# Optimization experiments

Hardware: AMD Instinct MI355X
Metric: run time of the kernel (lower is better)

The kernel has to match this reference:

```python
import jax, jax.numpy as jnp
import numpy as np

# static config matching init_kwargs / setup
T = 0.1      # temperature
MARG = 0.0   # margin m
NEG_IOU = 0.5
K = 1        # pos_topk
WEIGHT = 1.0
P = 2080     # number of True entries in mask2d (triu of 64x64)


def _normalize(x, axis=-1, eps=1e-12):
    n = jnp.sqrt(jnp.sum(x * x, axis=axis, keepdims=True))
    return x / jnp.maximum(n, eps)


def _log_ce(pos_scores, all_scores, neg_mask, t, m):
    # pos_scores: (..., K); all_scores: (..., K or 1, L); neg_mask broadcastable to all_scores
    pos_logit = (pos_scores - m) / t
    pos_exp = jnp.exp(pos_logit)
    neg_exp_sum = jnp.sum(jnp.exp(all_scores / t) * neg_mask.astype(all_scores.dtype), axis=-1)
    loss = -(pos_logit - jnp.log(pos_exp + neg_exp_sum))
    return jnp.mean(loss)


def setup_inputs() -> dict:
    key = jax.random.key(0)
    k1, k2, k3, k4 = jax.random.split(key, 4)
    S, C, N, B, M = 64, 256, 64, 16, 128
    video_feats = jax.random.normal(k1, (S, C, N, N), dtype=jnp.float32)
    sents_feats = jax.random.normal(k2, (S, C), dtype=jnp.float32)
    iou2d = jax.random.uniform(k3, (S, N, N), dtype=jnp.float32)
    iou2ds = jax.random.uniform(k4, (M, N, N), dtype=jnp.float32)
    num_sentences = jnp.full((B,), 4, dtype=jnp.int32)   # sum == S
    num_targets = jnp.full((S,), 2, dtype=jnp.int32)     # sum == M
    mask2d = jnp.triu(jnp.ones((N, N), dtype=bool))      # P = 2080 valid proposals
    return {
        "video_feats": video_feats, "sents_feats": sents_feats,
        "iou2d": iou2d, "iou2ds": iou2ds,
        "num_sentences": num_sentences, "num_targets": num_targets,
        "mask2d": mask2d,
    }


def reference(video_feats, sents_feats, iou2d, iou2ds, num_sentences, num_targets, mask2d):
    S, C, N, _ = video_feats.shape
    B = num_sentences.shape[0]
    M = iou2ds.shape[0]

    # flat proposal indices (static count P)
    mask_idx = jnp.nonzero(mask2d.reshape(-1), size=P)[0]

    # scatter maps
    scatter_b2s = jnp.concatenate([jnp.zeros((1,), jnp.int32),
                                   jnp.cumsum(num_sentences)[:-1].astype(jnp.int32)])  # (B,)
    scatter_m2s = jnp.repeat(jnp.arange(S), num_targets, total_repeat_length=M)        # (M,)
    scatter_s2b = jnp.repeat(jnp.arange(B), num_sentences, total_repeat_length=S)      # (S,)

    # select valid proposals: (S,C,P) -> (S,P,C)
    vf = video_feats.reshape(S, C, N * N)[:, :, mask_idx].transpose(0, 2, 1)
    iou2d_f = iou2d.reshape(S, N * N)[:, mask_idx]    # (S,P)
    iou2ds_f = iou2ds.reshape(M, N * N)[:, mask_idx]  # (M,P)

    vf = _normalize(vf, axis=-1)          # (S,P,C)
    sf = _normalize(sents_feats, axis=-1) # (S,C)

    # top-K proposals per moment
    topk_idxs = jax.lax.top_k(iou2ds_f, K)[1]                         # (M,K)
    allm_vf = vf[scatter_m2s]                                         # (M,P,C)
    topk_vf = jnp.take_along_axis(allm_vf, topk_idxs[:, :, None], 1)  # (M,K,C)

    # inter-video loss
    inter_video_pos = jnp.sum(topk_vf * sf[scatter_m2s][:, None, :], axis=-1)  # (M,K)
    inter_video_all = jnp.einsum('mkc,sc->mks', topk_vf, sf)                   # (M,K,S)
    eye_mask = ~jnp.eye(S, dtype=bool)
    inter_video_neg_mask = eye_mask[scatter_m2s][:, None, :]                   # (M,1,S)
    loss_inter_video = _log_ce(inter_video_pos, inter_video_all, inter_video_neg_mask, T, MARG)

    # inter-query loss
    inter_query_pos = inter_video_pos                                  # (M,K)
    vf_b = vf[scatter_b2s].reshape(B * P, C)                           # one sentence-rep per video
    inter_query_all = jnp.einsum('sc,qc->sq', sf, vf_b)[:, None, :]    # (S,1,B*P)

    # pos_mask: row s has its video block b=scatter_s2b[s] set to (iou2d > neg_iou)
    s2v_pos = iou2d_f > NEG_IOU                                        # (S,P)
    pos_mask = jnp.zeros((S, B, P), dtype=bool)
    pos_mask = pos_mask.at[jnp.arange(S), scatter_s2b].set(s2v_pos)
    pos_mask = pos_mask.reshape(S, B * P)
    inter_query_neg_mask = (~pos_mask)[:, None, :]                     # (S,1,B*P)

    loss_inter_query = _log_ce(inter_query_pos,
                               inter_query_all[scatter_m2s],
                               inter_query_neg_mask[scatter_m2s], T, MARG)

    return (loss_inter_video + loss_inter_query) * WEIGHT
```

## Files before the change

### kernel.cpp

```cpp
#include <hip/hip_runtime.h>
#include <math.h>

#define C 256
#define NN 4096
#define SDIM 64
#define T_INV 10.0f
#define NEG_IOU_TH 0.5f
#define QTILE 256
#define QTILES (NN / QTILE)

__device__ __forceinline__ float wave_reduce_sum(float v) {
    #pragma unroll
    for (int off = 32; off > 0; off >>= 1) v += __shfl_xor(v, off, 64);
    return v;
}

__global__ void k_prep(const float* __restrict__ sents,
                       const int* __restrict__ num_sentences,
                       const int* __restrict__ num_targets,
                       int B, int S, int M,
                       float* __restrict__ sfT, int* __restrict__ b2s,
                       int* __restrict__ s2b, int* __restrict__ m2s,
                       float* __restrict__ denomq, int* __restrict__ counter) {
    __shared__ float red[4];
    int s = blockIdx.x, tid = threadIdx.x;
    float v = sents[(size_t)s * C + tid];
    float ssq = wave_reduce_sum(v * v);
    int lane = tid & 63, wave = tid >> 6;
    if (lane == 0) red[wave] = ssq;
    __syncthreads();
    float tot = red[0] + red[1] + red[2] + red[3];
    sfT[(size_t)tid * S + s] = v * (1.0f / fmaxf(sqrtf(tot), 1e-12f));

    if (blockIdx.x == 0) {
        if (tid < S) denomq[tid] = 0.f;
        if (tid == 0) {
            *counter = 0;
            int acc = 0;
            for (int b = 0; b < B; ++b) {
                b2s[b] = acc;
                int nsb = num_sentences[b];
                for (int k = 0; k < nsb; ++k) s2b[acc + k] = b;
                acc += nsb;
            }
            int mi = 0;
            for (int si = 0; si < S; ++si) {
                int nt = num_targets[si];
                for (int k = 0; k < nt; ++k) m2s[mi++] = si;
            }
        }
    }
}

__global__ void __launch_bounds__(256)
k_main(const float* __restrict__ vf, const float* __restrict__ iou2d,
       const float* __restrict__ iou2ds, const int* __restrict__ num_sentences,
       const float* __restrict__ sfT, const int* __restrict__ b2s,
       const int* __restrict__ m2s,
       float* __restrict__ pos, float* __restrict__ negiv,
       float* __restrict__ denomq, int* __restrict__ counter,
       float* __restrict__ out, int S, int B, int M, int nq, int ntot) {
    __shared__ float sT[C * SDIM];
    __shared__ float red[4];
    __shared__ int   sidx[4];
    __shared__ float dw[4][SDIM];
    __shared__ int   bestflat;
    __shared__ int   amlast;

    int bid = blockIdx.x, tid = threadIdx.x;
    int lane = tid & 63, wave = tid >> 6;

    if (bid >= M) {
        int qb   = bid - M;
        int tile = qb & (QTILES - 1);
        int b    = qb >> 4;
        int sb = b2s[b];
        int ns = num_sentences[b];

        {
            const float4* src = (const float4*)sfT;
            float4* dst = (float4*)sT;
            #pragma unroll
            for (int k = 0; k < (C * SDIM) / (4 * 256); ++k)
                dst[tid + k * 256] = src[tid + k * 256];
        }
        __syncthreads();

        int flat = tile * QTILE + tid;
        const float* vp = vf + (size_t)sb * C * NN + flat;

        float acc[SDIM];
        #pragma unroll
        for (int s = 0; s < SDIM; ++s) acc[s] = 0.f;
        float ssq = 0.f;

        for (int c0 = 0; c0 < C; c0 += 4) {
            float v0 = vp[(size_t)(c0 + 0) * NN];
            float v1 = vp[(size_t)(c0 + 1) * NN];
            float v2 = vp[(size_t)(c0 + 2) * NN];
            float v3 = vp[(size_t)(c0 + 3) * NN];
            ssq += v0 * v0 + v1 * v1 + v2 * v2 + v3 * v3;
            #pragma unroll
            for (int j = 0; j < 4; ++j) {
                float v = (j == 0) ? v0 : (j == 1) ? v1 : (j == 2) ? v2 : v3;
                const float4* sr = (const float4*)&sT[(c0 + j) * SDIM];
                #pragma unroll
                for (int q4 = 0; q4 < SDIM / 4; ++q4) {
                    float4 s4 = sr[q4];
                    acc[q4 * 4 + 0] += s4.x * v;
                    acc[q4 * 4 + 1] += s4.y * v;
                    acc[q4 * 4 + 2] += s4.z * v;
                    acc[q4 * 4 + 3] += s4.w * v;
                }
            }
        }

        int r = flat >> 6, cc = flat & 63;
        bool valid = (cc >= r);
        float scale = (1.0f / fmaxf(sqrtf(ssq), 1e-12f)) * T_INV;

        unsigned long long excl = 0ull;
        for (int i = 0; i < ns; ++i)
            if (iou2d[(size_t)(sb + i) * NN + flat] > NEG_IOU_TH)
                excl |= (1ull << (sb + i));
        if (!valid) excl = ~0ull;

        #pragma unroll
        for (int s = 0; s < SDIM; ++s) {
            float e = ((excl >> s) & 1ull) ? 0.f : expf(acc[s] * scale);
            e = wave_reduce_sum(e);
            if (lane == 0) dw[wave][s] = e;
        }
        __syncthreads();
        if (tid < SDIM)
            atomicAdd(&denomq[tid],
                      dw[0][tid] + dw[1][tid] + dw[2][tid] + dw[3][tid]);
    } else {
        int m = bid;
        int s_m = m2s[m];
        float* tv  = sT;
        float* sc4 = sT + C;

        float bv = -1e30f; int bi = NN;
        #pragma unroll
        for (int j = 0; j < NN / 256; ++j) {
            int flat = tid + j * 256;
            int rr = flat >> 6, cc = flat & 63;
            if (cc >= rr) {
                float val = iou2ds[(size_t)m * NN + flat];
                if (val > bv || (val == bv && flat < bi)) { bv = val; bi = flat; }
            }
        }
        #pragma unroll
        for (int off = 32; off > 0; off >>= 1) {
            float ov = __shfl_xor(bv, off, 64);
            int   oi = __shfl_xor(bi, off, 64);
            if (ov > bv || (ov == bv && oi < bi)) { bv = ov; bi = oi; }
        }
        if (lane == 0) { red[wave] = bv; sidx[wave] = bi; }
        __syncthreads();
        if (tid == 0) {
            float v0 = red[0]; int i0 = sidx[0];
            for (int w = 1; w < 4; ++w)
                if (red[w] > v0 || (red[w] == v0 && sidx[w] < i0)) { v0 = red[w]; i0 = sidx[w]; }
            bestflat = i0;
        }
        __syncthreads();
        int flat = bestflat;

        float v = vf[((size_t)s_m * C + tid) * NN + flat];
        float ssq = wave_reduce_sum(v * v);
        if (lane == 0) red[wave] = ssq;
        __syncthreads();
        float tot = red[0] + red[1] + red[2] + red[3];
        tv[tid] = v * (1.0f / fmaxf(sqrtf(tot), 1e-12f));
        __syncthreads();

        {
            int s = tid & 63, cg = tid >> 6;
            float d = 0.f;
            for (int j = 0; j < 64; ++j) {
                int c2 = cg * 64 + j;
                d += tv[c2] * sfT[(size_t)c2 * S + s];
            }
            sc4[cg * 64 + s] = d;
        }
        __syncthreads();
        if (tid < 64) {
            float d = sc4[tid] + sc4[64 + tid] + sc4[128 + tid] + sc4[192 + tid];
            if (tid == s_m) atomicExch(&pos[m], d);
            float e = (tid == s_m) ? 0.f : expf(d * T_INV);
            e = wave_reduce_sum(e);
            if (tid == 0) atomicExch(&negiv[m], e);
        }
    }

    __syncthreads();
    if (tid == 0) {
        __threadfence();
        int old = atomicAdd(counter, 1);
        amlast = (old == ntot - 1) ? 1 : 0;
    }
    __syncthreads();
    if (!amlast) return;

    __threadfence();
    float val = 0.f;
    for (int m = tid; m < M; m += 256) {
        int s = m2s[m];
        float pl  = atomicAdd(&pos[m], 0.f) * T_INV;
        float niv = atomicAdd(&negiv[m], 0.f);
        float dq  = atomicAdd(&denomq[s], 0.f);
        float pe = expf(pl);
        val += -(pl - logf(pe + niv)) + -(pl - logf(pe + dq));
    }
    val = wave_reduce_sum(val);
    if (lane == 0) dw[0][wave] = val;
    __syncthreads();
    if (tid == 0) out[0] = (dw[0][0] + dw[0][1] + dw[0][2] + dw[0][3]) / (float)M;
}

extern "C" void kernel_launch(void* const* d_in, const int* in_sizes, int n_in,
                              void* d_out, int out_size, void* d_ws, size_t ws_size,
                              hipStream_t stream) {
    const float* video_feats   = (const float*)d_in[0];
    const float* sents_feats   = (const float*)d_in[1];
    const float* iou2d         = (const float*)d_in[2];
    const float* iou2ds        = (const float*)d_in[3];
    const int*   num_sentences = (const int*)d_in[4];
    const int*   num_targets   = (const int*)d_in[5];

    const int S = in_sizes[2] / NN;
    const int B = in_sizes[4];
    const int M = in_sizes[3] / NN;

    float* sfT    = (float*)d_ws;
    float* pos    = sfT + (size_t)C * 64;
    float* negiv  = pos + M;
    float* denomq = negiv + M;
    int*   b2s    = (int*)(denomq + S);
    int*   s2b    = b2s + B;
    int*   m2s    = s2b + S;
    int*   counter = m2s + M;

    const int nq   = QTILES * B;
    const int ntot = M + nq;

    k_prep<<<S, C, 0, stream>>>(sents_feats, num_sentences, num_targets,
                                B, S, M, sfT, b2s, s2b, m2s, denomq, counter);
    k_main<<<ntot, 256, 0, stream>>>(video_feats, iou2d, iou2ds, num_sentences,
                                     sfT, b2s, m2s, pos, negiv, denomq, counter,
                                     (float*)d_out, S, B, M, nq, ntot);
}
```

Measured before the change: 405.9 us.

## Split sentence dimension across blocks and drop LDS staging of sentence features

Each query-tile block now handles 32 of the 64 sentences, which doubles the grid and halves the per-thread accumulator registers. Sentence features are read straight from global memory, where every lane reads the same address, instead of first copying 64KB into LDS. The per-sentence wave reductions are replaced by a butterfly transpose-reduce over shuffles. The cost is that video features are read twice, once per sentence group, and the decode of b hardcodes B=16.

```diff
diff --git a/kernel.cpp b/kernel.cpp
--- a/kernel.cpp
+++ b/kernel.cpp
@@ -6,6 +6,7 @@
 #define SDIM 64
 #define T_INV 10.0f
 #define NEG_IOU_TH 0.5f
+#define SG 32
 #define QTILE 256
 #define QTILES (NN / QTILE)
 
@@ -60,12 +61,13 @@
        float* __restrict__ pos, float* __restrict__ negiv,
        float* __restrict__ denomq, int* __restrict__ counter,
        float* __restrict__ out, int S, int B, int M, int nq, int ntot) {
-    __shared__ float sT[C * SDIM];
     __shared__ float red[4];
     __shared__ int   sidx[4];
     __shared__ float dw[4][SDIM];
     __shared__ int   bestflat;
     __shared__ int   amlast;
+    __shared__ float tv[C];
+    __shared__ float sc4[256];
 
     int bid = blockIdx.x, tid = threadIdx.x;
     int lane = tid & 63, wave = tid >> 6;
@@ -73,45 +75,33 @@
     if (bid >= M) {
         int qb   = bid - M;
         int tile = qb & (QTILES - 1);
-        int b    = qb >> 4;
+        int rem  = qb >> 4;
+        int b    = rem & 15;
+        int g    = rem >> 4;
         int sb = b2s[b];
         int ns = num_sentences[b];
 
-        {
-            const float4* src = (const float4*)sfT;
-            float4* dst = (float4*)sT;
-            #pragma unroll
-            for (int k = 0; k < (C * SDIM) / (4 * 256); ++k)
-                dst[tid + k * 256] = src[tid + k * 256];
-        }
-        __syncthreads();
-
         int flat = tile * QTILE + tid;
         const float* vp = vf + (size_t)sb * C * NN + flat;
-
-        float acc[SDIM];
-        #pragma unroll
-        for (int s = 0; s < SDIM; ++s) acc[s] = 0.f;
+        const float4* sq = (const float4*)sfT + (size_t)g * 8;
+
+        float acc[SG];
+        #pragma unroll
+        for (int s = 0; s < SG; ++s) acc[s] = 0.f;
         float ssq = 0.f;
 
-        for (int c0 = 0; c0 < C; c0 += 4) {
-            float v0 = vp[(size_t)(c0 + 0) * NN];
-            float v1 = vp[(size_t)(c0 + 1) * NN];
-            float v2 = vp[(size_t)(c0 + 2) * NN];
-            float v3 = vp[(size_t)(c0 + 3) * NN];
-            ssq += v0 * v0 + v1 * v1 + v2 * v2 + v3 * v3;
+        #pragma unroll 4
+        for (int c = 0; c < C; ++c) {
+            float v = vp[(size_t)c * NN];
+            ssq += v * v;
+            const float4* sqc = sq + (size_t)c * (SDIM / 4);
             #pragma unroll
-            for (int j = 0; j < 4; ++j) {
-                float v = (j == 0) ? v0 : (j == 1) ? v1 : (j == 2) ? v2 : v3;
-                const float4* sr = (const float4*)&sT[(c0 + j) * SDIM];
-                #pragma unroll
-                for (int q4 = 0; q4 < SDIM / 4; ++q4) {
-                    float4 s4 = sr[q4];
-                    acc[q4 * 4 + 0] += s4.x * v;
-                    acc[q4 * 4 + 1] += s4.y * v;
-                    acc[q4 * 4 + 2] += s4.z * v;
-                    acc[q4 * 4 + 3] += s4.w * v;
-                }
+            for (int k = 0; k < SG / 4; ++k) {
+                float4 q4 = sqc[k];
+                acc[k * 4 + 0] += q4.x * v;
+                acc[k * 4 + 1] += q4.y * v;
+                acc[k * 4 + 2] += q4.z * v;
+                acc[k * 4 + 3] += q4.w * v;
             }
         }
 
@@ -125,21 +115,30 @@
                 excl |= (1ull << (sb + i));
         if (!valid) excl = ~0ull;
 
-        #pragma unroll
-        for (int s = 0; s < SDIM; ++s) {
-            float e = ((excl >> s) & 1ull) ? 0.f : expf(acc[s] * scale);
-            e = wave_reduce_sum(e);
-            if (lane == 0) dw[wave][s] = e;
-        }
-        __syncthreads();
-        if (tid < SDIM)
-            atomicAdd(&denomq[tid],
+        unsigned mask32 = (unsigned)(excl >> (g * 32));
+        #pragma unroll
+        for (int i = 0; i < SG; ++i)
+            acc[i] = ((mask32 >> i) & 1u) ? 0.f : expf(acc[i] * scale);
+
+        #pragma unroll
+        for (int off = 16; off >= 1; off >>= 1) {
+            int bsel = lane & off;
+            #pragma unroll
+            for (int i = 0; i < off; ++i) {
+                float keep = bsel ? acc[off + i] : acc[i];
+                float send = bsel ? acc[i] : acc[off + i];
+                acc[i] = keep + __shfl_xor(send, off, 64);
+            }
+        }
+        float tot_s = acc[0] + __shfl_xor(acc[0], 32, 64);
+        if (lane < 32) dw[wave][lane] = tot_s;
+        __syncthreads();
+        if (tid < 32)
+            atomicAdd(&denomq[g * 32 + tid],
                       dw[0][tid] + dw[1][tid] + dw[2][tid] + dw[3][tid]);
     } else {
         int m = bid;
         int s_m = m2s[m];
-        float* tv  = sT;
-        float* sc4 = sT + C;
 
         float bv = -1e30f; int bi = NN;
         #pragma unroll
@@ -243,7 +242,7 @@
     int*   m2s    = s2b + S;
     int*   counter = m2s + M;
 
-    const int nq   = QTILES * B;
+    const int nq   = QTILES * B * (SDIM / SG);
     const int ntot = M + nq;
 
     k_prep<<<S, C, 0, stream>>>(sents_feats, num_sentences, num_targets,
```

Result: faster. 383.7 us (-5.5%).
